# Optimization experiments

Hardware: AMD Instinct MI355X
Metric: run time of the kernel (lower is better)

## Reference

```python
import jax, jax.numpy as jnp
import numpy as np

RADII = (3, 5, 7)      # window_levels
S, B, D = 1024, 8, 512  # seq_len, batch, feature_dim
EPS = 1e-12             # F.normalize eps


def setup_inputs() -> dict:
    key = jax.random.key(0)
    k0, k1, k2 = jax.random.split(key, 3)
    x = jax.random.normal(k0, (S, B, D), jnp.float32)          # seq-first like the torch path
    W = jax.random.normal(k1, (3, D, D), jnp.float32) / np.sqrt(D)  # 3 level linear weights
    b = jax.random.normal(k2, (3, D), jnp.float32) * 0.01           # 3 level linear biases
    alphas = jnp.ones((3,), jnp.float32)   # nn.Parameter(torch.ones)
    betas = jnp.zeros((3,), jnp.float32)   # nn.Parameter(torch.zeros)
    return {"x": x, "W": W, "b": b, "alphas": alphas, "betas": betas}


def reference(x, W, b, alphas, betas):
    # x: [S, B, D] (seq-first). torch code transposes to [B, S, D], works, transposes back.
    # Dropout is identity (eval mode). output = x + sum over levels of per-timestep
    # windowed, similarity-weighted sums of linearly transformed neighbors; all
    # windows read the ORIGINAL x, so levels are independent additive terms.
    xb = jnp.transpose(x, (1, 0, 2))  # [B, S, D]
    Bn, Sn, Dn = xb.shape
    dt = xb.dtype
    # L2-normalized features (F.normalize with eps=1e-12)
    xnorm = xb / jnp.maximum(jnp.linalg.norm(xb, axis=-1, keepdims=True), EPS)
    # prefix sums for O(1) window means (edge-truncated windows)
    csum = jnp.concatenate([jnp.zeros((Bn, 1, Dn), dt), jnp.cumsum(xb, axis=1)], axis=1)
    t_idx = jnp.arange(Sn)
    out = xb
    for m, r in enumerate(RADII):
        starts = jnp.clip(t_idx - r, 0, Sn)        # [S]
        ends = jnp.clip(t_idx + r + 1, 0, Sn)      # [S]
        cnt = (ends - starts).astype(dt)           # window sizes (truncated at edges)
        center = (csum[:, ends, :] - csum[:, starts, :]) / cnt[None, :, None]  # [B,S,D]
        cnorm = center / jnp.maximum(jnp.linalg.norm(center, axis=-1, keepdims=True), EPS)
        # sliding-window gather indices, masked at sequence edges
        offs = jnp.arange(-r, r + 1)
        pos = t_idx[:, None] + offs[None, :]       # [S, w]
        valid = ((pos >= 0) & (pos < Sn)).astype(dt)
        idx = jnp.clip(pos, 0, Sn - 1)
        nw = xnorm[:, idx, :]                      # [B, S, w, D]
        sim = jnp.einsum('bswd,bsd->bsw', nw, cnorm)  # cosine similarity to window mean
        wts = jax.nn.sigmoid(alphas[m] * sim + betas[m]) * valid[None, :, :]
        tfm = xb @ W[m].T + b[m]                   # level-m linear transform, computed once
        tw = tfm[:, idx, :]                        # [B, S, w, D]
        out = out + jnp.einsum('bsw,bswd->bsd', wts, tw)
    return jnp.transpose(out, (1, 0, 2))  # back to [S, B, D]
```

## Files before the change

kernel.cpp:

```cpp
#include <hip/hip_runtime.h>

typedef __attribute__((ext_vector_type(8))) short short8;
typedef __attribute__((ext_vector_type(4))) float f32x4;

#define S_LEN 1024
#define B_N 8
#define D_DIM 512
#define SLAB 4194304
#define NX   4194304

static __device__ __forceinline__ unsigned short f2bf(float f){
  unsigned int u = __float_as_uint(f);
  u = u + 0x7fffu + ((u>>16)&1u);
  return (unsigned short)(u>>16);
}
static __device__ __forceinline__ float bf2f(unsigned short h){
  return __uint_as_float(((unsigned int)h)<<16);
}
static __device__ __forceinline__ ushort4 cvt4(float4 v){
  ushort4 h; h.x=f2bf(v.x); h.y=f2bf(v.y); h.z=f2bf(v.z); h.w=f2bf(v.w); return h;
}

#define GLL16(g,l) __builtin_amdgcn_global_load_lds( \
    (__attribute__((address_space(1))) void*)(g), \
    (__attribute__((address_space(3))) void*)(l), 16, 0, 0)

#define SBAR() do { __builtin_amdgcn_sched_barrier(0); \
  asm volatile("s_barrier" ::: "memory"); \
  __builtin_amdgcn_sched_barrier(0); } while(0)
#define VMCNT(n) asm volatile("s_waitcnt vmcnt(" #n ")" ::: "memory")

__global__ __launch_bounds__(256) void k_conv(const float* __restrict__ x,
    const float* __restrict__ W, unsigned short* __restrict__ xbf,
    unsigned short* __restrict__ wbf)
{
  int tid = blockIdx.x*256 + threadIdx.x;
  const float4* xs = (const float4*)x;
  ushort4* xd = (ushort4*)xbf;
  float4 v0 = xs[tid];
  float4 v1 = xs[tid + 262144];
  float4 v2 = xs[tid + 524288];
  float4 v3 = xs[tid + 786432];
  xd[tid         ] = cvt4(v0);
  xd[tid + 262144] = cvt4(v1);
  xd[tid + 524288] = cvt4(v2);
  xd[tid + 786432] = cvt4(v3);
  if (tid < 196608){
    const float4* ws_ = (const float4*)W;
    ushort4* wd = (ushort4*)wbf;
    wd[tid] = cvt4(ws_[tid]);
  }
}

__global__ __launch_bounds__(256) void k_heavy(const unsigned short* __restrict__ A,
    const unsigned short* __restrict__ Bw, const float* __restrict__ bias,
    unsigned short* __restrict__ C, float* __restrict__ Gband)
{
  __shared__ __align__(16) unsigned short smem[24576];
  int blk = blockIdx.x;
  int tid = threadIdx.x, lane = tid & 63, w = tid >> 6;

  if (blk >= 768){
    int g = blk - 768;
    int b = g & 7, i0 = (g >> 3) * 16;
    #pragma unroll
    for (int q = 0; q < 12; ++q){
      int r = w*12 + q;
      int t = i0 - 16 + r;
      t = t < 0 ? 0 : (t > S_LEN-1 ? S_LEN-1 : t);
      const unsigned short* src = A + ((size_t)(t*B_N + b))*512 + ((lane ^ (r & 7))*8);
      GLL16(src, smem + r*512);
    }
    __syncthreads();
    int j0 = i0 + (w - 1) * 16;
    if (w < 3 && j0 >= 0 && j0 < S_LEN){
      int l15 = lane & 15;
      int cbase = lane >> 4;
      int sw = l15 & 7;
      f32x4 acc = (f32x4){0.f,0.f,0.f,0.f};
      #pragma unroll
      for (int kt = 0; kt < 16; ++kt){
        int ch = (kt*4 + cbase) ^ sw;
        short8 af = *(const short8*)(smem + (16 + l15)*512 + ch*8);
        short8 bf = *(const short8*)(smem + (w*16 + l15)*512 + ch*8);
        acc = __builtin_amdgcn_mfma_f32_16x16x32_bf16(af, bf, acc, 0,0,0);
      }
      int rb = (lane >> 4) * 4;
      #pragma unroll
      for (int rg = 0; rg < 4; ++rg){
        int i = i0 + rb + rg;
        int dl = j0 + l15 - i;
        if (dl >= -14 && dl <= 14)
          Gband[((size_t)b * S_LEN + i) * 32 + dl + 14] = acc[rg];
      }
    }
    return;
  }

  int xcd = blk & 7, ixc = blk >> 3;
  int by = xcd * 8 + ixc / 12;
  int bx = ixc % 12;
  int wm = w >> 1, wn = w & 1;
  int c0 = w*128 + lane, c1 = c0 + 64;
  const unsigned short* gA0 = A + (size_t)(by*128 + (c0>>2))*512 + (c0&3)*8;
  const unsigned short* gA1 = A + (size_t)(by*128 + (c1>>2))*512 + (c1&3)*8;
  const unsigned short* gB0 = Bw + (size_t)(bx*128 + (c0>>2))*512 + (c0&3)*8;
  const unsigned short* gB1 = Bw + (size_t)(bx*128 + (c1>>2))*512 + (c1&3)*8;
  f32x4 acc[4][4];
  #pragma unroll
  for (int i=0;i<4;++i)
    #pragma unroll
    for (int j=0;j<4;++j)
      acc[i][j] = (f32x4){0.f,0.f,0.f,0.f};
  int l15 = lane & 15, klo = (lane>>4)*8;
  {
    unsigned short* s0 = smem + w*1024;
    GLL16(gA0, s0); GLL16(gA1, s0 + 512);
    GLL16(gB0, s0 + 4096); GLL16(gB1, s0 + 4096 + 512);
    gA0 += 32; gA1 += 32; gB0 += 32; gB1 += 32;
    unsigned short* s1 = smem + 8192 + w*1024;
    GLL16(gA0, s1); GLL16(gA1, s1 + 512);
    GLL16(gB0, s1 + 4096); GLL16(gB1, s1 + 4096 + 512);
    gA0 += 32; gA1 += 32; gB0 += 32; gB1 += 32;
  }
  VMCNT(4); SBAR();
  #pragma unroll
  for (int kt = 0; kt < 16; ++kt){
    unsigned short* sc = smem + (kt % 3)*8192;
    if (kt + 2 < 16){
      unsigned short* sn = smem + ((kt + 2) % 3)*8192 + w*1024;
      GLL16(gA0, sn); GLL16(gA1, sn + 512);
      GLL16(gB0, sn + 4096); GLL16(gB1, sn + 4096 + 512);
      gA0 += 32; gA1 += 32; gB0 += 32; gB1 += 32;
    }
    short8 af[4], bfr[4];
    #pragma unroll
    for (int i=0;i<4;++i)
      af[i] = *(const short8*)(sc + (wm*64 + i*16 + l15)*32 + klo);
    #pragma unroll
    for (int j=0;j<4;++j)
      bfr[j] = *(const short8*)(sc + 4096 + (wn*64 + j*16 + l15)*32 + klo);
    #pragma unroll
    for (int i=0;i<4;++i)
      #pragma unroll
      for (int j=0;j<4;++j)
        acc[i][j] = __builtin_amdgcn_mfma_f32_16x16x32_bf16(af[i], bfr[j], acc[i][j], 0,0,0);
    if (kt < 15){
      __builtin_amdgcn_sched_barrier(0);
      if (kt + 2 < 16){ VMCNT(4); }
      else            { VMCNT(0); }
      SBAR();
    }
  }
  __syncthreads();
  int rbase = (lane>>4)*4;
  #pragma unroll
  for (int j=0;j<4;++j){
    int nl = wn*64 + j*16 + l15;
    float bv = bias[bx*128 + nl];
    #pragma unroll
    for (int i=0;i<4;++i){
      int rl0 = wm*64 + i*16 + rbase;
      #pragma unroll
      for (int rg=0;rg<4;++rg)
        smem[(rl0+rg)*128 + nl] = f2bf(acc[i][j][rg] + bv);
    }
  }
  __syncthreads();
  int m_r = bx >> 2, colb = (bx&3)*128;
  #pragma unroll
  for (int p=0;p<8;++p){
    int R = p*16 + (tid>>4);
    int ch = (tid&15)*8;
    uint4 v = *(const uint4*)(smem + R*128 + ch);
    *(uint4*)(C + (size_t)m_r*SLAB + (size_t)(by*128 + R)*512 + colb + ch) = v;
  }
}

__global__ __launch_bounds__(256) void k_gath(const float* __restrict__ x,
    const unsigned short* __restrict__ tfm, const float* __restrict__ Gband,
    const float* __restrict__ alphas, const float* __restrict__ betas,
    float* __restrict__ out)
{
  int blk = blockIdx.x;
  int b = blk & 7, tg = blk >> 3;
  int tid = threadIdx.x, h = tid >> 7, j = tid & 127;
  int t = tg * 2 + h;
  int d0 = j * 4;
  size_t xoff = ((size_t)t * B_N + b) * D_DIM + d0;
  float4 a = *(const float4*)(x + xoff);
  __shared__ float pshare[2][33];
  __shared__ float invc[2][3];
  __shared__ float wsh[2][33];
  int m = 0, pos = 0, valid = 0;
  float pp = 0.f, invnp = 0.f;
  if (j < 33){
    int r, wsl;
    if (j < 7){ m = 0; r = 3; wsl = j; }
    else if (j < 18){ m = 1; r = 5; wsl = j - 7; }
    else { m = 2; r = 7; wsl = j - 18; }
    pos = t + wsl - r;
    valid = (pos >= 0 && pos < S_LEN);
    if (valid){
      const float* grow = Gband + ((size_t)b * S_LEN + pos) * 32;
      int ulo = max(t - r, 0), uhi = min(t + r, S_LEN - 1);
      for (int uu = ulo; uu <= uhi; ++uu) pp += grow[uu - pos + 14];
      invnp = rsqrtf(fmaxf(grow[14], 1e-24f));
    }
    pshare[h][j] = valid ? pp : 0.f;
  }
  __syncthreads();
  if (j < 3){
    int s0 = j == 0 ? 0 : (j == 1 ? 7 : 18);
    int c  = j == 0 ? 7 : (j == 1 ? 11 : 15);
    float s = 0.f;
    for (int k = 0; k < c; ++k) s += pshare[h][s0 + k];
    invc[h][j] = rsqrtf(fmaxf(s, 1e-24f));
  }
  __syncthreads();
  if (j < 33){
    float wt = 0.f;
    if (valid){
      float sim = pp * invnp * invc[h][m];
      float z = alphas[m] * sim + betas[m];
      wt = 1.0f / (1.0f + expf(-z));
    }
    wsh[h][j] = wt;
  }
  __syncthreads();
  float ax = a.x, ay = a.y, az = a.z, aw = a.w;
  #pragma unroll
  for (int p = 0; p < 33; ++p){
    int pm, pr, wsl;
    if (p < 7){ pm = 0; pr = 3; wsl = p; }
    else if (p < 18){ pm = 1; pr = 5; wsl = p - 7; }
    else { pm = 2; pr = 7; wsl = p - 18; }
    int ppos = t + wsl - pr;
    if (ppos < 0 || ppos >= S_LEN) continue;
    float wt = wsh[h][p];
    const unsigned short* tp = tfm + (size_t)pm * SLAB + ((size_t)ppos * B_N + b) * D_DIM + d0;
    uint2 uv = *(const uint2*)tp;
    ax += wt * bf2f((unsigned short)(uv.x & 0xffffu));
    ay += wt * bf2f((unsigned short)(uv.x >> 16));
    az += wt * bf2f((unsigned short)(uv.y & 0xffffu));
    aw += wt * bf2f((unsigned short)(uv.y >> 16));
  }
  *(float4*)(out + xoff) = make_float4(ax, ay, az, aw);
}

extern "C" void kernel_launch(void* const* d_in, const int* in_sizes, int n_in,
                              void* d_out, int out_size, void* d_ws, size_t ws_size,
                              hipStream_t stream) {
  const float* x      = (const float*)d_in[0];
  const float* W      = (const float*)d_in[1];
  const float* bias   = (const float*)d_in[2];
  const float* alphas = (const float*)d_in[3];
  const float* betas  = (const float*)d_in[4];
  float* out = (float*)d_out;
  char* ws = (char*)d_ws;
  unsigned short* xbf  = (unsigned short*)ws;
  unsigned short* wbf  = (unsigned short*)(ws + 8388608);
  unsigned short* tfm  = (unsigned short*)(ws + 8388608 + 1572864);
  float*          Gband= (float*)(ws + 8388608 + 1572864 + 25165824);

  k_conv <<<1024, 256, 0, stream>>>(x, W, xbf, wbf);
  k_heavy<<<1280, 256, 0, stream>>>(xbf, wbf, bias, tfm, Gband);
  k_gath <<<4096, 256, 0, stream>>>(x, tfm, Gband, alphas, betas, out);
}
```

Before: 59.96 us.

## Enlarge GEMM tile to 256x256 with 512 threads and swizzled LDS

Rewrites the fused GEMM kernel to use 256x256 output tiles computed by 8 waves (512 threads), with a K-step of 64 and double buffering in place of the previous 128x128 tile with triple buffering. LDS is XOR-swizzled to avoid bank conflicts, MFMA sections are bracketed with s_setprio, and the epilogue staging also uses swizzled addresses. The grid shrinks from 1280 to 704 blocks and the band-Gram blocks are spread over 8 waves. The aim is more data reuse per LDS load and fewer global reloads of A and B. In exchange it uses 128KB of LDS per block and far fewer GEMM blocks (192), which risks poor occupancy and load imbalance across CUs.

```diff
diff --git a/kernel.cpp b/kernel.cpp
--- a/kernel.cpp
+++ b/kernel.cpp
@@ -52,20 +52,21 @@
   }
 }
 
-__global__ __launch_bounds__(256) void k_heavy(const unsigned short* __restrict__ A,
+__global__ __launch_bounds__(512, 2) void k_heavy(const unsigned short* __restrict__ A,
     const unsigned short* __restrict__ Bw, const float* __restrict__ bias,
     unsigned short* __restrict__ C, float* __restrict__ Gband)
 {
-  __shared__ __align__(16) unsigned short smem[24576];
+  __shared__ __align__(16) unsigned short smem[65536];
   int blk = blockIdx.x;
   int tid = threadIdx.x, lane = tid & 63, w = tid >> 6;
-
-  if (blk >= 768){
-    int g = blk - 768;
+  int l15 = lane & 15, l4 = lane >> 4;
+
+  if (blk >= 192){
+    int g = blk - 192;
     int b = g & 7, i0 = (g >> 3) * 16;
     #pragma unroll
-    for (int q = 0; q < 12; ++q){
-      int r = w*12 + q;
+    for (int q = 0; q < 6; ++q){
+      int r = w*6 + q;
       int t = i0 - 16 + r;
       t = t < 0 ? 0 : (t > S_LEN-1 ? S_LEN-1 : t);
       const unsigned short* src = A + ((size_t)(t*B_N + b))*512 + ((lane ^ (r & 7))*8);
@@ -74,18 +75,16 @@
     __syncthreads();
     int j0 = i0 + (w - 1) * 16;
     if (w < 3 && j0 >= 0 && j0 < S_LEN){
-      int l15 = lane & 15;
-      int cbase = lane >> 4;
       int sw = l15 & 7;
       f32x4 acc = (f32x4){0.f,0.f,0.f,0.f};
       #pragma unroll
       for (int kt = 0; kt < 16; ++kt){
-        int ch = (kt*4 + cbase) ^ sw;
+        int ch = (kt*4 + l4) ^ sw;
         short8 af = *(const short8*)(smem + (16 + l15)*512 + ch*8);
         short8 bf = *(const short8*)(smem + (w*16 + l15)*512 + ch*8);
         acc = __builtin_amdgcn_mfma_f32_16x16x32_bf16(af, bf, acc, 0,0,0);
       }
-      int rb = (lane >> 4) * 4;
+      int rb = l4 * 4;
       #pragma unroll
       for (int rg = 0; rg < 4; ++rg){
         int i = i0 + rb + rg;
@@ -97,83 +96,99 @@
     return;
   }
 
-  int xcd = blk & 7, ixc = blk >> 3;
-  int by = xcd * 8 + ixc / 12;
-  int bx = ixc % 12;
-  int wm = w >> 1, wn = w & 1;
-  int c0 = w*128 + lane, c1 = c0 + 64;
-  const unsigned short* gA0 = A + (size_t)(by*128 + (c0>>2))*512 + (c0&3)*8;
-  const unsigned short* gA1 = A + (size_t)(by*128 + (c1>>2))*512 + (c1&3)*8;
-  const unsigned short* gB0 = Bw + (size_t)(bx*128 + (c0>>2))*512 + (c0&3)*8;
-  const unsigned short* gB1 = Bw + (size_t)(bx*128 + (c1>>2))*512 + (c1&3)*8;
-  f32x4 acc[4][4];
-  #pragma unroll
-  for (int i=0;i<4;++i)
-    #pragma unroll
-    for (int j=0;j<4;++j)
-      acc[i][j] = (f32x4){0.f,0.f,0.f,0.f};
-  int l15 = lane & 15, klo = (lane>>4)*8;
-  {
-    unsigned short* s0 = smem + w*1024;
-    GLL16(gA0, s0); GLL16(gA1, s0 + 512);
-    GLL16(gB0, s0 + 4096); GLL16(gB1, s0 + 4096 + 512);
-    gA0 += 32; gA1 += 32; gB0 += 32; gB1 += 32;
-    unsigned short* s1 = smem + 8192 + w*1024;
-    GLL16(gA0, s1); GLL16(gA1, s1 + 512);
-    GLL16(gB0, s1 + 4096); GLL16(gB1, s1 + 4096 + 512);
-    gA0 += 32; gA1 += 32; gB0 += 32; gB1 += 32;
-  }
-  VMCNT(4); SBAR();
-  #pragma unroll
-  for (int kt = 0; kt < 16; ++kt){
-    unsigned short* sc = smem + (kt % 3)*8192;
-    if (kt + 2 < 16){
-      unsigned short* sn = smem + ((kt + 2) % 3)*8192 + w*1024;
-      GLL16(gA0, sn); GLL16(gA1, sn + 512);
-      GLL16(gB0, sn + 4096); GLL16(gB1, sn + 4096 + 512);
-      gA0 += 32; gA1 += 32; gB0 += 32; gB1 += 32;
-    }
-    short8 af[4], bfr[4];
-    #pragma unroll
-    for (int i=0;i<4;++i)
-      af[i] = *(const short8*)(sc + (wm*64 + i*16 + l15)*32 + klo);
-    #pragma unroll
-    for (int j=0;j<4;++j)
-      bfr[j] = *(const short8*)(sc + 4096 + (wn*64 + j*16 + l15)*32 + klo);
-    #pragma unroll
-    for (int i=0;i<4;++i)
-      #pragma unroll
-      for (int j=0;j<4;++j)
-        acc[i][j] = __builtin_amdgcn_mfma_f32_16x16x32_bf16(af[i], bfr[j], acc[i][j], 0,0,0);
-    if (kt < 15){
-      __builtin_amdgcn_sched_barrier(0);
-      if (kt + 2 < 16){ VMCNT(4); }
-      else            { VMCNT(0); }
-      SBAR();
-    }
-  }
-  __syncthreads();
-  int rbase = (lane>>4)*4;
-  #pragma unroll
-  for (int j=0;j<4;++j){
-    int nl = wn*64 + j*16 + l15;
-    float bv = bias[bx*128 + nl];
-    #pragma unroll
-    for (int i=0;i<4;++i){
-      int rl0 = wm*64 + i*16 + rbase;
-      #pragma unroll
-      for (int rg=0;rg<4;++rg)
-        smem[(rl0+rg)*128 + nl] = f2bf(acc[i][j][rg] + bv);
-    }
-  }
-  __syncthreads();
-  int m_r = bx >> 2, colb = (bx&3)*128;
-  #pragma unroll
-  for (int p=0;p<8;++p){
-    int R = p*16 + (tid>>4);
-    int ch = (tid&15)*8;
-    uint4 v = *(const uint4*)(smem + R*128 + ch);
-    *(uint4*)(C + (size_t)m_r*SLAB + (size_t)(by*128 + R)*512 + colb + ch) = v;
+  int xcd = blk & 7, ic = blk >> 3;
+  int by = xcd*4 + ic/6, bx = ic % 6;
+  int wm = w >> 2, wn = w & 3;
+  const unsigned short* ga[4];
+  const unsigned short* gb[4];
+  #pragma unroll
+  for (int q = 0; q < 4; ++q){
+    int c = q*512 + tid;
+    int row = c >> 3, col8 = (c & 7) ^ (row & 7);
+    ga[q] = A  + (size_t)(by*256 + row)*512 + col8*8;
+    gb[q] = Bw + (size_t)(bx*256 + row)*512 + col8*8;
+  }
+  f32x4 acc[8][4];
+  #pragma unroll
+  for (int i2=0;i2<8;++i2)
+    #pragma unroll
+    for (int j2=0;j2<4;++j2)
+      acc[i2][j2] = (f32x4){0.f,0.f,0.f,0.f};
+
+#define STAGE(bsel) do{ \
+    unsigned short* sb_ = smem + (bsel)*32768; \
+    _Pragma("unroll") for (int q_=0;q_<4;++q_){ GLL16(ga[q_], sb_ + (q_*512 + w*64)*8); ga[q_] += 64; } \
+    _Pragma("unroll") for (int q_=0;q_<4;++q_){ GLL16(gb[q_], sb_ + 16384 + (q_*512 + w*64)*8); gb[q_] += 64; } \
+  }while(0)
+
+  STAGE(0); STAGE(1);
+  VMCNT(8); SBAR();
+  int swk = l15 & 7;
+  for (int kt = 0; kt < 8; ++kt){
+    const unsigned short* Ab = smem + (kt&1)*32768;
+    const unsigned short* Bb = Ab + 16384;
+    short8 bfr[4][2];
+    #pragma unroll
+    for (int nf=0;nf<4;++nf)
+      #pragma unroll
+      for (int kk=0;kk<2;++kk){
+        int brow = wn*64 + nf*16 + l15;
+        bfr[nf][kk] = *(const short8*)(Bb + (brow*8 + ((kk*4 + l4) ^ swk))*8);
+      }
+    #pragma unroll
+    for (int qm=0;qm<2;++qm){
+      short8 afr[4][2];
+      #pragma unroll
+      for (int i2=0;i2<4;++i2)
+        #pragma unroll
+        for (int kk=0;kk<2;++kk){
+          int arow = wm*128 + qm*64 + i2*16 + l15;
+          afr[i2][kk] = *(const short8*)(Ab + (arow*8 + ((kk*4 + l4) ^ swk))*8);
+        }
+      __builtin_amdgcn_s_setprio(1);
+      #pragma unroll
+      for (int i2=0;i2<4;++i2)
+        #pragma unroll
+        for (int nf=0;nf<4;++nf)
+          #pragma unroll
+          for (int kk=0;kk<2;++kk)
+            acc[qm*4+i2][nf] = __builtin_amdgcn_mfma_f32_16x16x32_bf16(
+                afr[i2][kk], bfr[nf][kk], acc[qm*4+i2][nf], 0,0,0);
+      __builtin_amdgcn_s_setprio(0);
+    }
+    SBAR();
+    if (kt + 2 < 8){ STAGE(kt&1); VMCNT(8); }
+    else           { VMCNT(0); }
+    SBAR();
+  }
+#undef STAGE
+
+  __syncthreads();
+  #pragma unroll
+  for (int nf=0;nf<4;++nf){
+    float bv = bias[bx*256 + wn*64 + nf*16 + l15];
+    int col = wn*64 + nf*16 + l15;
+    #pragma unroll
+    for (int mf=0;mf<8;++mf){
+      int row0 = wm*128 + mf*16 + l4*4;
+      #pragma unroll
+      for (int k=0;k<4;++k){
+        int row = row0 + k;
+        unsigned int boff = ((unsigned int)row*512u + (unsigned int)col*2u) ^ (((unsigned int)row&7u)<<4);
+        *(unsigned short*)((char*)smem + boff) = f2bf(acc[mf][nf][k] + bv);
+      }
+    }
+  }
+  __syncthreads();
+  #pragma unroll
+  for (int it=0; it<16; ++it){
+    int gch = tid + it*512;
+    int row = gch >> 5, cc = gch & 31;
+    unsigned int boff = ((unsigned int)row*512u + (unsigned int)cc*16u) ^ (((unsigned int)row&7u)<<4);
+    uint4 v = *(const uint4*)((char*)smem + boff);
+    int grow = by*256 + row, gcol = bx*256 + cc*8;
+    int m_r = gcol >> 9, c512 = gcol & 511;
+    *(uint4*)(C + (size_t)m_r*SLAB + (size_t)grow*512 + c512) = v;
   }
 }
 
@@ -264,6 +279,6 @@
   float*          Gband= (float*)(ws + 8388608 + 1572864 + 25165824);
 
   k_conv <<<1024, 256, 0, stream>>>(x, W, xbf, wbf);
-  k_heavy<<<1280, 256, 0, stream>>>(xbf, wbf, bias, tfm, Gband);
+  k_heavy<<< 704, 512, 0, stream>>>(xbf, wbf, bias, tfm, Gband);
   k_gath <<<4096, 256, 0, stream>>>(x, tfm, Gband, alphas, betas, out);
 }
```

Result: slower. 65.95 us (+10.0%).
